# Kernel tuning notes

Hardware: AMD Instinct MI355X
Metric: run time of the kernel (lower is better)

Reference implementation:

```python
import jax, jax.numpy as jnp
import numpy as np

NEG = -1e20  # finite stand-in for -inf (exp underflows to 0; avoids nan grads)
S_RANGE = 19   # prune_range hard-coded in the module
TERM = 0       # termination/blank symbol
LM_ONLY = 0.25 # lm_only_scale; am_only_scale = 0 so that branch vanishes


def _mi(px, py):
    """RNN-T mutual-information forward DP (fast_rnnt mutual_information_recursion).
    px: (B,S,T+1) logprob of emitting symbol s+1 at (s,t); py: (B,S+1,T) blank logprobs.
    p[b,s,t] = logaddexp(p[b,s-1,t]+px[b,s-1,t], p[b,s,t-1]+py[b,s,t-1]); returns p[:,S,T]."""
    B, S, T1 = px.shape
    p0 = jnp.concatenate([jnp.zeros((B, 1), px.dtype),
                          jnp.cumsum(py[:, 0, :], axis=1)], axis=1)  # row s=0: (B,T+1)
    def outer(p_prev, inp):
        px_s, py_s = inp                 # (B,T+1), (B,T)
        b = p_prev + px_s                # vertical (emit) path into next row
        def inner(c, xs):
            b_t, py_t = xs
            c = jnp.logaddexp(b_t, c + py_t)
            return c, c
        _, rest = jax.lax.scan(inner, b[:, 0], (b[:, 1:].T, py_s.T))  # rest: (T,B)
        p_row = jnp.concatenate([b[:, :1], rest.T], axis=1)
        return p_row, None
    p_last, _ = jax.lax.scan(outer, p0,
                             (jnp.moveaxis(px, 1, 0), jnp.moveaxis(py[:, 1:, :], 1, 0)))
    return p_last[:, -1]  # (B,) total log-prob at (S,T)


def _smoothed_logprobs(am, lm, symbols):
    """fast_rnnt.get_rnnt_logprobs_smoothed with lm_only_scale=0.25, am_only_scale=0."""
    B, T, C = am.shape
    S = symbols.shape[1]
    lm_max = jnp.max(lm, axis=2, keepdims=True)   # (B,S+1,1)
    am_max = jnp.max(am, axis=2, keepdims=True)   # (B,T,1)
    lm_p = jnp.exp(lm - lm_max)
    am_p = jnp.exp(am - am_max)
    # normalizers[b,s,t] = log sum_k exp(lm[b,s,k] + am[b,t,k]) via matmul trick
    normalizers = jnp.log(jnp.einsum('bsc,btc->bst', lm_p, am_p)) \
        + lm_max + jnp.swapaxes(am_max, 1, 2)     # (B,S+1,T)
    sym_b = jnp.broadcast_to(symbols[:, None, :], (B, T, S))
    px_am = jnp.swapaxes(jnp.take_along_axis(am, sym_b, axis=2), 1, 2)  # (B,S,T)
    px_lm = jnp.take_along_axis(lm[:, :S], symbols[:, :, None], axis=2)  # (B,S,1)
    px = px_am + px_lm - normalizers[:, :S, :]
    lm_lsm = jax.nn.log_softmax(lm, axis=2)
    px_lmonly = jnp.take_along_axis(lm_lsm[:, :S], symbols[:, :, None], axis=2)
    comb = 1.0 - LM_ONLY
    px_i = comb * px + LM_ONLY * px_lmonly
    px_i = jnp.concatenate([px_i, jnp.full((B, S, 1), NEG, px_i.dtype)], axis=2)  # (B,S,T+1)
    py = am[:, :, TERM][:, None, :] + lm[:, :, TERM][:, :, None] - normalizers
    py_i = comb * py + LM_ONLY * lm_lsm[:, :, TERM][:, :, None]  # (B,S+1,T)
    return px_i, py_i


def _suffix_min(x):  # fast_rnnt _monotonic_lower_bound: x[t] = min(x[t:])
    return jax.lax.associative_scan(jnp.minimum, x, axis=1, reverse=True)


def _adjust_lower_bound(s_begin, r):  # fast_rnnt _adjust_pruning_lower_bound
    Tn = s_begin.shape[1]
    s_begin = _suffix_min(s_begin)
    off = (r - 1) * jnp.arange(Tn, dtype=s_begin.dtype)
    y = -(s_begin - off)
    y = jnp.maximum(_suffix_min(y), 0)
    return -(y - off)


def _prune_ranges(px_grad, py_grad, r):
    """fast_rnnt.get_rnnt_prune_ranges (all sequences full length)."""
    B, S, T1 = px_grad.shape
    T = T1 - 1
    py_pad = jnp.concatenate([py_grad, jnp.zeros((B, S + 1, 1), py_grad.dtype)], axis=2)
    tot = jnp.concatenate([px_grad, jnp.zeros((B, 1, T1), px_grad.dtype)], axis=1) + py_pad
    tot = jnp.concatenate([jnp.zeros((B, 1, T1), tot.dtype), tot], axis=1)  # (B,S+2,T1)
    cs = jnp.cumsum(tot, axis=1)
    diff = cs[:, r:, :] - cs[:, :-r, :]  # windowed occupancy sums
    s_begin = jnp.argmax(diff, axis=1)[:, :T].astype(jnp.int32)
    s_begin = _adjust_lower_bound(s_begin, r)
    return s_begin[:, :, None] + jnp.arange(r, dtype=jnp.int32)[None, None, :]  # (B,T,r)


def _pruned_logprobs(logits, symbols, ranges):
    """fast_rnnt.get_rnnt_logprobs_pruned."""
    B, T, r, C = logits.shape
    S = symbols.shape[1]
    norm = jax.nn.logsumexp(logits, axis=3)  # (B,T,r)
    sym_t = jnp.concatenate([symbols, jnp.full((B, 1), TERM, symbols.dtype)], axis=1)
    sym_b = jnp.broadcast_to(sym_t[:, None, :], (B, T, S + 1))
    pruned_sym = jnp.take_along_axis(sym_b, ranges, axis=2)  # (B,T,r)
    px = jnp.take_along_axis(logits, pruned_sym[..., None], axis=3)[..., 0] - norm
    py = logits[..., TERM] - norm
    def to_full(x):  # scatter (B,T,r) band into absolute symbol positions (B,T,S+1)
        pad = jnp.full((B, T, S + 1 - r), NEG, x.dtype)
        xf = jnp.concatenate([x, pad], axis=2)
        idx = (jnp.arange(S + 1)[None, None, :] - ranges[:, :, 0:1]) % (S + 1)
        return jnp.take_along_axis(xf, idx, axis=2)
    px_f = jnp.swapaxes(to_full(px), 1, 2)  # (B,S+1,T)
    py_f = jnp.swapaxes(to_full(py), 1, 2)  # (B,S+1,T)
    px_f = jnp.concatenate([px_f, jnp.full((B, S + 1, 1), NEG, px_f.dtype)], axis=2)[:, :S, :]
    return px_f, py_f  # (B,S,T+1), (B,S+1,T)


def _forward(am, lm, targets, joiner_w, joiner_b):
    px, py = _smoothed_logprobs(am, lm, targets)
    simple_loss = -jnp.mean(_mi(px, py))  # reduction='mean'
    # occupation-probability grads (values only, used for pruning)
    gpx, gpy = jax.grad(lambda a: jnp.sum(_mi(a[0], a[1])))(
        (jax.lax.stop_gradient(px), jax.lax.stop_gradient(py)))
    ranges = _prune_ranges(gpx, gpy, S_RANGE)  # (B,T,19) int32, constant wrt grads
    lm_pruned = jax.vmap(lambda l, rg: l[rg])(lm, ranges)  # (B,T,r,C) gather
    # joiner: logits = Linear(tanh(am_pruned + lm_pruned)); am broadcast over r
    logits = jnp.einsum('btrc,cd->btrd',
                        jnp.tanh(am[:, :, None, :] + lm_pruned), joiner_w) + joiner_b
    px2, py2 = _pruned_logprobs(logits.astype(jnp.float32), targets, ranges)
    pruned_loss = -jnp.mean(_mi(px2, py2))
    return 0.1 * simple_loss + pruned_loss


def setup_inputs() -> dict:
    key = jax.random.key(0)
    k = jax.random.split(key, 5)
    B, T, S, C = 8, 512, 128, 512
    return {
        "am": jax.random.normal(k[0], (B, T, C), jnp.float32),
        "lm": jax.random.normal(k[1], (B, S + 1, C), jnp.float32),
        "targets": jax.random.randint(k[2], (B, S), 1, C),  # blank=0 excluded
        "y_lens": jnp.full((B,), S, jnp.int32),             # full-length boundaries
        "joiner_w": 0.05 * jax.random.normal(k[3], (C, C), jnp.float32),
        "joiner_b": jnp.zeros((C,), jnp.float32),
    }


def reference(am, lm, targets, y_lens, joiner_w, joiner_b):
    # boundary = [0, 0, y_lens(=S), T] for every sequence
    return _forward(am, lm, targets, joiner_w, joiner_b)
```

## Files before the change

### kernel.cpp

```cpp
#include <hip/hip_runtime.h>
#include <math.h>

#define NEGV -1e20f
#define DPAD 132
#define RBOFF 16
#define ROWSA 676
#define RB(p,b) ((p) + ((size_t)(b) * ROWSA + RBOFF) * DPAD)
#define NROWS 77824

typedef __attribute__((ext_vector_type(4))) float floatx4;
typedef __attribute__((ext_vector_type(8))) short short8;


__device__ __forceinline__ float lae(float a, float b){
  float mx = fmaxf(a, b);
  float mn = fminf(a, b);
  return mx + __logf(1.f + __expf(mn - mx));
}

__device__ __forceinline__ short f2bf(float x){
  union { float f; unsigned u; } v; v.f = x;
  unsigned r = v.u + 0x7fffu + ((v.u >> 16) & 1u);
  return (short)(r >> 16);
}

__device__ __forceinline__ float tanh5(float x){
  float e = __expf(2.f * x);
  return 1.f - 2.f * __builtin_amdgcn_rcpf(e + 1.f);
}

__global__ __launch_bounds__(256) void k_row_stats(
    const float* __restrict__ in, float* __restrict__ outMax, float* __restrict__ outLse)
{
  int row = blockIdx.x;
  const float* r = in + (size_t)row * 512;
  int tid = threadIdx.x;
  float v0 = r[tid], v1 = r[tid + 256];
  float m = fmaxf(v0, v1);
  #pragma unroll
  for (int off = 32; off; off >>= 1) m = fmaxf(m, __shfl_xor(m, off, 64));
  __shared__ float sm[4];
  __shared__ float sbm;
  int wv = tid >> 6;
  if ((tid & 63) == 0) sm[wv] = m;
  __syncthreads();
  if (tid == 0) sbm = fmaxf(fmaxf(sm[0], sm[1]), fmaxf(sm[2], sm[3]));
  __syncthreads();
  float mx = sbm;
  if (tid == 0) outMax[row] = mx;
  if (outLse){
    float s = __expf(v0 - mx) + __expf(v1 - mx);
    #pragma unroll
    for (int off = 32; off; off >>= 1) s += __shfl_xor(s, off, 64);
    __shared__ float sp[4];
    if ((tid & 63) == 0) sp[wv] = s;
    __syncthreads();
    if (tid == 0) outLse[row] = mx + __logf(sp[0] + sp[1] + sp[2] + sp[3]);
  }
}

__global__ __launch_bounds__(256) void k_wb(const float* __restrict__ W, short* __restrict__ Wb){
  int idx = blockIdx.x * 256 + threadIdx.x;
  int d = idx >> 9, c = idx & 511;
  Wb[idx] = f2bf(W[c * 512 + d]);
}

__global__ __launch_bounds__(256) void k_norm(
    const float* __restrict__ am, const float* __restrict__ lm,
    const float* __restrict__ lmMax, const float* __restrict__ amMax,
    float* __restrict__ normv)
{
  int b = blockIdx.z;
  int s0 = blockIdx.y * 16;
  int t0 = blockIdx.x * 128;
  __shared__ float lmS[16][68];
  __shared__ float amS[128][68];
  int tid = threadIdx.x;
  int ts = tid >> 4, tt = tid & 15;
  float acc[8];
  #pragma unroll
  for (int j = 0; j < 8; ++j) acc[j] = 0.f;

  for (int k0 = 0; k0 < 512; k0 += 64){
    {
      int e = tid * 4;
      int rr = e >> 6, cc = e & 63;
      int s = s0 + rr;
      floatx4 o = {0.f, 0.f, 0.f, 0.f};
      if (s < 129){
        float mx = lmMax[b * 129 + s];
        floatx4 v = *(const floatx4*)(lm + ((size_t)(b * 129 + s)) * 512 + k0 + cc);
        o[0] = __expf(v[0] - mx); o[1] = __expf(v[1] - mx);
        o[2] = __expf(v[2] - mx); o[3] = __expf(v[3] - mx);
      }
      *(floatx4*)&lmS[rr][cc] = o;
    }
    #pragma unroll
    for (int i = 0; i < 8; ++i){
      int e = (tid + i * 256) * 4;
      int rr = e >> 6, cc = e & 63;
      float mx = amMax[b * 512 + t0 + rr];
      floatx4 v = *(const floatx4*)(am + ((size_t)(b * 512 + t0 + rr)) * 512 + k0 + cc);
      floatx4 o;
      o[0] = __expf(v[0] - mx); o[1] = __expf(v[1] - mx);
      o[2] = __expf(v[2] - mx); o[3] = __expf(v[3] - mx);
      *(floatx4*)&amS[rr][cc] = o;
    }
    __syncthreads();
    #pragma unroll 4
    for (int k = 0; k < 64; ++k){
      float a = lmS[ts][k];
      #pragma unroll
      for (int j = 0; j < 8; ++j) acc[j] += a * amS[tt + 16 * j][k];
    }
    __syncthreads();
  }
  int s = s0 + ts;
  if (s < 129){
    float lmx = lmMax[b * 129 + s];
    #pragma unroll
    for (int j = 0; j < 8; ++j){
      int t = t0 + tt + 16 * j;
      normv[((size_t)(b * 129 + s)) * 512 + t] = __logf(acc[j]) + lmx + amMax[b * 512 + t];
    }
  }
}

__global__ __launch_bounds__(256) void k_pxpy(
    const float* __restrict__ am, const float* __restrict__ lm,
    const int* __restrict__ targets, const float* __restrict__ normv,
    const float* __restrict__ lmLse, float* __restrict__ pxd, float* __restrict__ pyd)
{
  int bs = blockIdx.x;
  int b = bs / 129, s = bs % 129;
  float lm0 = lm[(size_t)bs * 512];
  float lse = lmLse[bs];
  int sym = 0; float lms = 0.f;
  if (s < 128){ sym = targets[b * 128 + s]; lms = lm[(size_t)bs * 512 + sym]; }
  const float* nrm = normv + (size_t)bs * 512;
  float* pydb = RB(pyd, b);
  float* pxdb = RB(pxd, b);
  for (int t = threadIdx.x; t < 513; t += 256){
    if (t < 512){
      float n = nrm[t];
      float a0 = am[((size_t)(b * 512 + t)) * 512];
      pydb[(size_t)(s + t) * DPAD + s] = 0.75f * (a0 + lm0 - n) + 0.25f * (lm0 - lse);
      if (s < 128){
        float as = am[((size_t)(b * 512 + t)) * 512 + sym];
        pxdb[(size_t)(s + t) * DPAD + s] = 0.75f * (as + lms - n) + 0.25f * (lms - lse);
      }
    } else if (s < 128){
      pxdb[(size_t)(s + 512) * DPAD + s] = NEGV;
    }
  }
}


__device__ __forceinline__ void dp_fwd_run(
    const float* __restrict__ pxb, const float* __restrict__ pyb,
    float* __restrict__ pab, float* __restrict__ tot, int b)
{
  int l = threadIdx.x;
  const int a = 2 * l;
  float curA = NEGV, curB = NEGV, curC = NEGV, send = NEGV;
  int paddr = (l - 1) << 2;

  float2 cpx = *(const float2*)(pxb - DPAD + a);
  float2 cpy = *(const float2*)(pyb - DPAD + a);
  float  cpz = pyb[-DPAD + 128];

  float2 b0px[8], b0py[8], b1px[8], b1py[8];
  float  b0pz[8], b1pz[8];
  float  outx[8], outy[8], outc[8];

  #pragma unroll
  for (int j = 0; j < 8; ++j){
    b0px[j] = *(const float2*)(pxb + (size_t)j * DPAD + a);
    b0py[j] = *(const float2*)(pyb + (size_t)j * DPAD + a);
    b0pz[j] = pyb[(size_t)j * DPAD + 128];
  }

  for (int i = 0; i < 40; ++i){
    int d0 = i * 16;
    #pragma unroll
    for (int j = 0; j < 8; ++j){
      b1px[j] = *(const float2*)(pxb + (size_t)(d0 + 8 + j) * DPAD + a);
      b1py[j] = *(const float2*)(pyb + (size_t)(d0 + 8 + j) * DPAD + a);
      b1pz[j] = pyb[(size_t)(d0 + 8 + j) * DPAD + 128];
    }
    #pragma unroll
    for (int j = 0; j < 8; ++j){
      int d = d0 + j;
      float2 pxm = j ? b0px[j - 1] : cpx;
      float2 pym = j ? b0py[j - 1] : cpy;
      float  pzm = j ? b0pz[j - 1] : cpz;
      float recv = __int_as_float(
          __builtin_amdgcn_ds_bpermute(paddr, __float_as_int(send)));
      int tA = d - a, tC = d - 128;
      float aaA = (l > 0) ? recv : NEGV;
      float bbA = (tA >= 1) ? curA + pym.x : NEGV;
      float nvA = lae(aaA, bbA);
      if (l == 0 && d == 0) nvA = 0.f;
      float aaB = curA + pxm.x;
      float bbB = (tA >= 2) ? curB + pym.y : NEGV;
      float nvB = lae(aaB, bbB);
      float aaC = curB + pxm.y;
      float bbC = (tC >= 1) ? curC + pzm : NEGV;
      float nvC = lae(aaC, bbC);
      if (tA >= 0 && tA <= 512) curA = nvA;
      if (tA >= 1 && tA <= 513) curB = nvB;
      if (tC >= 0 && tC <= 512) curC = nvC;
      send = curB + b0px[j].y;
      outx[j] = curA; outy[j] = curB; outc[j] = curC;
    }
    cpx = b0px[7]; cpy = b0py[7]; cpz = b0pz[7];
    if (pab){
      #pragma unroll
      for (int j = 0; j < 8; ++j)
        *(float2*)(pab + (size_t)(d0 + j) * DPAD + a) = make_float2(outx[j], outy[j]);
      if (l == 63){
        #pragma unroll
        for (int j = 0; j < 8; ++j)
          pab[(size_t)(d0 + j) * DPAD + 128] = outc[j];
      }
    }
    #pragma unroll
    for (int j = 0; j < 8; ++j){
      b0px[j] = *(const float2*)(pxb + (size_t)(d0 + 16 + j) * DPAD + a);
      b0py[j] = *(const float2*)(pyb + (size_t)(d0 + 16 + j) * DPAD + a);
      b0pz[j] = pyb[(size_t)(d0 + 16 + j) * DPAD + 128];
    }
    #pragma unroll
    for (int j = 0; j < 8; ++j){
      int d = d0 + 8 + j;
      float2 pxm = j ? b1px[j - 1] : cpx;
      float2 pym = j ? b1py[j - 1] : cpy;
      float  pzm = j ? b1pz[j - 1] : cpz;
      float recv = __int_as_float(
          __builtin_amdgcn_ds_bpermute(paddr, __float_as_int(send)));
      int tA = d - a, tC = d - 128;
      float aaA = (l > 0) ? recv : NEGV;
      float bbA = (tA >= 1) ? curA + pym.x : NEGV;
      float nvA = lae(aaA, bbA);
      float aaB = curA + pxm.x;
      float bbB = (tA >= 2) ? curB + pym.y : NEGV;
      float nvB = lae(aaB, bbB);
      float aaC = curB + pxm.y;
      float bbC = (tC >= 1) ? curC + pzm : NEGV;
      float nvC = lae(aaC, bbC);
      if (tA >= 0 && tA <= 512) curA = nvA;
      if (tA >= 1 && tA <= 513) curB = nvB;
      if (tC >= 0 && tC <= 512) curC = nvC;
      send = curB + b1px[j].y;
      outx[j] = curA; outy[j] = curB; outc[j] = curC;
    }
    cpx = b1px[7]; cpy = b1py[7]; cpz = b1pz[7];
    if (pab){
      #pragma unroll
      for (int j = 0; j < 8; ++j)
        *(float2*)(pab + (size_t)(d0 + 8 + j) * DPAD + a) = make_float2(outx[j], outy[j]);
      if (l == 63){
        #pragma unroll
        for (int j = 0; j < 8; ++j)
          pab[(size_t)(d0 + 8 + j) * DPAD + 128] = outc[j];
      }
    }
  }
  {
    float aaC = curB + cpx.y;
    float bbC = curC + cpz;
    curC = lae(aaC, bbC);
    if (l == 63){
      if (pab) pab[(size_t)640 * DPAD + 128] = curC;
      tot[b] = curC;
    }
  }
}

__device__ __forceinline__ void dp_bwd_run(
    const float* __restrict__ pxb, const float* __restrict__ pyb,
    float* __restrict__ beb)
{
  int l = threadIdx.x;
  const int a = 2 * l;
  float curA = NEGV, curB = NEGV, curC = NEGV, send = NEGV;
  int paddr = (l + 1) << 2;

  float2 b0px[8], b0py[8], b1px[8], b1py[8];
  float  b0pz[8], b1pz[8];
  float  outx[8], outy[8], outc[8];

  #pragma unroll
  for (int j = 0; j < 8; ++j){
    b0px[j] = *(const float2*)(pxb + (size_t)(640 - j) * DPAD + a);
    b0py[j] = *(const float2*)(pyb + (size_t)(640 - j) * DPAD + a);
    b0pz[j] = pyb[(size_t)(640 - j) * DPAD + 128];
  }

  for (int i = 0; i < 40; ++i){
    int d0 = 640 - 16 * i;
    #pragma unroll
    for (int j = 0; j < 8; ++j){
      b1px[j] = *(const float2*)(pxb + (size_t)(d0 - 8 - j) * DPAD + a);
      b1py[j] = *(const float2*)(pyb + (size_t)(d0 - 8 - j) * DPAD + a);
      b1pz[j] = pyb[(size_t)(d0 - 8 - j) * DPAD + 128];
    }
    #pragma unroll
    for (int j = 0; j < 8; ++j){
      int d = d0 - j;
      float2 pxA = b0px[j]; float2 pyA = b0py[j]; float pzA = b0pz[j];
      float recv = __int_as_float(
          __builtin_amdgcn_ds_bpermute(paddr, __float_as_int(send)));
      int tA = d - a, tB = tA - 1, tC = d - 128;
      float aaA = pxA.x + curB;
      float bbA = (tA <= 511) ? pyA.x + curA : NEGV;
      float nvA = lae(aaA, bbA);
      float up = (l < 63) ? recv : curC;
      float aaB = pxA.y + up;
      float bbB = (tB <= 511) ? pyA.y + curB : NEGV;
      float nvB = lae(aaB, bbB);
      float nvC = (tC <= 511) ? pzA + curC : NEGV;
      if (tC == 512) nvC = 0.f;
      if (tA >= 0 && tA <= 512) curA = nvA;
      if (tB >= 0 && tB <= 512) curB = nvB;
      if (tC >= 0 && tC <= 512) curC = nvC;
      send = curA;
      outx[j] = curA; outy[j] = curB; outc[j] = curC;
    }
    #pragma unroll
    for (int j = 0; j < 8; ++j)
      *(float2*)(beb + (size_t)(d0 - j) * DPAD + a) = make_float2(outx[j], outy[j]);
    if (l == 63){
      #pragma unroll
      for (int j = 0; j < 8; ++j)
        beb[(size_t)(d0 - j) * DPAD + 128] = outc[j];
    }
    #pragma unroll
    for (int j = 0; j < 8; ++j){
      b0px[j] = *(const float2*)(pxb + (size_t)(d0 - 16 - j) * DPAD + a);
      b0py[j] = *(const float2*)(pyb + (size_t)(d0 - 16 - j) * DPAD + a);
      b0pz[j] = pyb[(size_t)(d0 - 16 - j) * DPAD + 128];
    }
    #pragma unroll
    for (int j = 0; j < 8; ++j){
      int d = d0 - 8 - j;
      float2 pxA = b1px[j]; float2 pyA = b1py[j]; float pzA = b1pz[j];
      float recv = __int_as_float(
          __builtin_amdgcn_ds_bpermute(paddr, __float_as_int(send)));
      int tA = d - a, tB = tA - 1, tC = d - 128;
      float aaA = pxA.x + curB;
      float bbA = (tA <= 511) ? pyA.x + curA : NEGV;
      float nvA = lae(aaA, bbA);
      float up = (l < 63) ? recv : curC;
      float aaB = pxA.y + up;
      float bbB = (tB <= 511) ? pyA.y + curB : NEGV;
      float nvB = lae(aaB, bbB);
      float nvC = (tC <= 511) ? pzA + curC : NEGV;
      if (tC == 512) nvC = 0.f;
      if (tA >= 0 && tA <= 512) curA = nvA;
      if (tB >= 0 && tB <= 512) curB = nvB;
      if (tC >= 0 && tC <= 512) curC = nvC;
      send = curA;
      outx[j] = curA; outy[j] = curB; outc[j] = curC;
    }
    #pragma unroll
    for (int j = 0; j < 8; ++j)
      *(float2*)(beb + (size_t)(d0 - 8 - j) * DPAD + a) = make_float2(outx[j], outy[j]);
    if (l == 63){
      #pragma unroll
      for (int j = 0; j < 8; ++j)
        beb[(size_t)(d0 - 8 - j) * DPAD + 128] = outc[j];
    }
  }
  {
    float2 pxA = b0px[0]; float2 pyA = b0py[0];
    float recv = __int_as_float(
        __builtin_amdgcn_ds_bpermute(paddr, __float_as_int(send)));
    int tA = -a, tB = tA - 1;
    float aaA = pxA.x + curB;
    float bbA = (tA <= 511) ? pyA.x + curA : NEGV;
    float nvA = lae(aaA, bbA);
    float up = (l < 63) ? recv : curC;
    float aaB = pxA.y + up;
    float bbB = (tB <= 511) ? pyA.y + curB : NEGV;
    float nvB = lae(aaB, bbB);
    if (tA >= 0 && tA <= 512) curA = nvA;
    if (tB >= 0 && tB <= 512) curB = nvB;
    *(float2*)(beb + a) = make_float2(curA, curB);
    if (l == 63) beb[128] = curC;
  }
}

__global__ __launch_bounds__(64) void k_dp_fb(
    const float* __restrict__ pxd, const float* __restrict__ pyd,
    float* __restrict__ pad, float* __restrict__ betad, float* __restrict__ tots)
{
  int blk = blockIdx.x;
  if (blk < 8){
    int b = blk;
    dp_fwd_run(RB(pxd, b), RB(pyd, b), RB(pad, b), tots, b);
  } else {
    int b = blk - 8;
    dp_bwd_run(RB(pxd, b), RB(pyd, b), RB(betad, b));
  }
}

__global__ __launch_bounds__(64) void k_dp_f2(
    const float* __restrict__ pxd, const float* __restrict__ pyd,
    float* __restrict__ totp)
{
  int b = blockIdx.x;
  dp_fwd_run(RB(pxd, b), RB(pyd, b), (float*)nullptr, totp, b);
}

__global__ __launch_bounds__(256) void k_window(
    const float* __restrict__ pxd, const float* __restrict__ pyd,
    const float* __restrict__ pad, const float* __restrict__ betad,
    const float* __restrict__ tots, int* __restrict__ sbr)
{
  __shared__ float tote[129][66];
  int b = blockIdx.x >> 3;
  int t0 = (blockIdx.x & 7) << 6;
  const float* px = RB(pxd, b);
  const float* py = RB(pyd, b);
  const float* pa = RB(pad, b);
  const float* be = RB(betad, b);
  float tv = tots[b];
  int tid = threadIdx.x;
  int wv = tid >> 6, ln = tid & 63;
  for (int dd = wv; dd < 192; dd += 4){
    int d = t0 + dd;
    int slo = dd - 63 > 0 ? dd - 63 : 0;
    int shi = dd < 128 ? dd : 128;
    int s = slo + ln;
    if (s <= shi){
      size_t r0 = (size_t)d * DPAD + s, r1 = (size_t)(d + 1) * DPAD + s;
      float pav = pa[r0];
      float v = __expf(pav + py[r0] + be[r1] - tv);
      if (s < 128) v += __expf(pav + px[r0] + be[r1 + 1] - tv);
      tote[s][dd - s] = v;
    }
  }
  __syncthreads();
  if (tid < 64){
    int c = tid;
    float win = 0.f;
    for (int s = 0; s < 19; ++s) win += tote[s][c];
    float best = win; int arg = 0;
    for (int w2 = 1; w2 <= 110; ++w2){
      win += tote[w2 + 18][c] - tote[w2 - 1][c];
      if (win > best){ best = win; arg = w2; }
    }
    sbr[b * 512 + t0 + c] = arg;
  }
}

__global__ void k_adjust(const int* __restrict__ sbr, int* __restrict__ sbeg){
  if (threadIdx.x != 0) return;
  int b = blockIdx.x;
  const int* in = sbr + b * 512;
  int* out = sbeg + b * 512;
  int sbm = 1 << 30, ym = 1 << 30;
  for (int t = 511; t >= 0; --t){
    sbm = min(sbm, in[t]);
    int y = 18 * t - sbm;
    ym = min(ym, y);
    int yc = ym > 0 ? ym : 0;
    out[t] = 18 * t - yc;
  }
}

__global__ __launch_bounds__(256) void k_stageH(
    const float* __restrict__ am, const float* __restrict__ lm,
    const int* __restrict__ sbeg, short* __restrict__ Hb)
{
  __shared__ int rowAm[64], rowLm[64];
  int tid = threadIdx.x;
  int r0 = blockIdx.x * 64;
  if (tid < 64){
    int row = r0 + tid;
    int g = row / 19;
    int j = row - g * 19;
    int b = g >> 9, t = g & 511;
    int sidx = sbeg[b * 512 + t] + j;
    rowAm[tid] = (b * 512 + t) * 512;
    rowLm[tid] = (b * 129 + sidx) * 512;
  }
  __syncthreads();
  int row = tid >> 2;
  int kb = (tid & 3) * 8;
  const float* ap = am + (size_t)rowAm[row];
  const float* lp = lm + (size_t)rowLm[row];
  short* hp = Hb + (size_t)(r0 + row) * 512;
  #pragma unroll 4
  for (int i = 0; i < 16; ++i){
    int k = kb + i * 32;
    floatx4 a0 = *(const floatx4*)(ap + k);
    floatx4 a1 = *(const floatx4*)(ap + k + 4);
    floatx4 l0 = *(const floatx4*)(lp + k);
    floatx4 l1 = *(const floatx4*)(lp + k + 4);
    short8 h;
    h[0] = f2bf(tanh5(a0[0] + l0[0]));
    h[1] = f2bf(tanh5(a0[1] + l0[1]));
    h[2] = f2bf(tanh5(a0[2] + l0[2]));
    h[3] = f2bf(tanh5(a0[3] + l0[3]));
    h[4] = f2bf(tanh5(a1[0] + l1[0]));
    h[5] = f2bf(tanh5(a1[1] + l1[1]));
    h[6] = f2bf(tanh5(a1[2] + l1[2]));
    h[7] = f2bf(tanh5(a1[3] + l1[3]));
    *(short8*)(hp + k) = h;
  }
}

__global__ __launch_bounds__(256) void k_jgemm(
    const short* __restrict__ Hb, const short* __restrict__ Wb,
    const float* __restrict__ bias, const int* __restrict__ targets,
    const int* __restrict__ sbeg,
    float2* __restrict__ pms, float* __restrict__ pxraw, float* __restrict__ pyraw)
{
  __shared__ int rowSym[128];
  __shared__ float redM[128][2];
  __shared__ float redS[128][2];
  __shared__ float rowM[128];

  int tid = threadIdx.x;
  int rt = blockIdx.x;
  int nb = blockIdx.y;
  int r0 = rt * 128, c0 = nb * 128;
  if (tid < 128){
    int row = r0 + tid;
    int g = row / 19;
    int j = row - g * 19;
    int b = g >> 9, t = g & 511;
    int sidx = sbeg[b * 512 + t] + j;
    rowSym[tid] = (sidx < 128) ? targets[b * 128 + sidx] : 0;
  }
  __syncthreads();

  int w = tid >> 6, lane = tid & 63, q = lane >> 4, ln = lane & 15;
  int mBase = (w & 1) * 64;
  int nBase = (w >> 1) * 64;
  const short* Ab = Hb + (size_t)(r0 + mBase + ln) * 512 + q * 8;
  const short* Bb = Wb + (size_t)(c0 + nBase + ln) * 512 + q * 8;

  floatx4 acc[4][4];
  #pragma unroll
  for (int mt = 0; mt < 4; ++mt)
    #pragma unroll
    for (int nt = 0; nt < 4; ++nt) acc[mt][nt] = (floatx4){0.f, 0.f, 0.f, 0.f};

  #pragma unroll 2
  for (int k0 = 0; k0 < 512; k0 += 32){
    short8 af[4], bf[4];
    #pragma unroll
    for (int mt = 0; mt < 4; ++mt)
      af[mt] = *(const short8*)(Ab + (size_t)mt * 16 * 512 + k0);
    #pragma unroll
    for (int nt = 0; nt < 4; ++nt)
      bf[nt] = *(const short8*)(Bb + (size_t)nt * 16 * 512 + k0);
    #pragma unroll
    for (int nt = 0; nt < 4; ++nt)
      #pragma unroll
      for (int mt = 0; mt < 4; ++mt)
        acc[mt][nt] = __builtin_amdgcn_mfma_f32_16x16x32_bf16(af[mt], bf[nt], acc[mt][nt], 0, 0, 0);
  }

  #pragma unroll
  for (int nt = 0; nt < 4; ++nt){
    int col = c0 + nBase + nt * 16 + ln;
    float bc = bias[col];
    #pragma unroll
    for (int mt = 0; mt < 4; ++mt)
      #pragma unroll
      for (int r = 0; r < 4; ++r){
        float v = acc[mt][nt][r] + bc;
        acc[mt][nt][r] = v;
        int rl = mBase + mt * 16 + q * 4 + r;
        if (col == 0) pyraw[r0 + rl] = v;
        if (col == rowSym[rl]) pxraw[r0 + rl] = v;
      }
  }
  #pragma unroll
  for (int mt = 0; mt < 4; ++mt)
    #pragma unroll
    for (int r = 0; r < 4; ++r){
      int rl = mBase + mt * 16 + q * 4 + r;
      float m = acc[mt][0][r];
      #pragma unroll
      for (int nt = 1; nt < 4; ++nt) m = fmaxf(m, acc[mt][nt][r]);
      m = fmaxf(m, __shfl_xor(m, 1, 16));
      m = fmaxf(m, __shfl_xor(m, 2, 16));
      m = fmaxf(m, __shfl_xor(m, 4, 16));
      m = fmaxf(m, __shfl_xor(m, 8, 16));
      if (ln == 0) redM[rl][w >> 1] = m;
    }
  __syncthreads();
  if (tid < 128) rowM[tid] = fmaxf(redM[tid][0], redM[tid][1]);
  __syncthreads();
  #pragma unroll
  for (int mt = 0; mt < 4; ++mt)
    #pragma unroll
    for (int r = 0; r < 4; ++r){
      int rl = mBase + mt * 16 + q * 4 + r;
      float rm = rowM[rl];
      float sa = 0.f;
      #pragma unroll
      for (int nt = 0; nt < 4; ++nt) sa += __expf(acc[mt][nt][r] - rm);
      sa += __shfl_xor(sa, 1, 16);
      sa += __shfl_xor(sa, 2, 16);
      sa += __shfl_xor(sa, 4, 16);
      sa += __shfl_xor(sa, 8, 16);
      if (ln == 0) redS[rl][w >> 1] = sa;
    }
  __syncthreads();
  if (tid < 128)
    pms[(size_t)nb * NROWS + r0 + tid] = make_float2(rowM[tid], redS[tid][0] + redS[tid][1]);
}

__global__ __launch_bounds__(256) void k_jfin(
    const float2* __restrict__ pms, const float* __restrict__ pxraw,
    const float* __restrict__ pyraw, float* __restrict__ pxv, float* __restrict__ pyv)
{
  int row = blockIdx.x * 256 + threadIdx.x;
  float2 p0 = pms[row];
  float2 p1 = pms[NROWS + row];
  float2 p2 = pms[2 * NROWS + row];
  float2 p3 = pms[3 * NROWS + row];
  float M = fmaxf(fmaxf(p0.x, p1.x), fmaxf(p2.x, p3.x));
  float S = p0.y * __expf(p0.x - M) + p1.y * __expf(p1.x - M)
          + p2.y * __expf(p2.x - M) + p3.y * __expf(p3.x - M);
  float norm = M + __logf(S);
  pxv[row] = pxraw[row] - norm;
  pyv[row] = pyraw[row] - norm;
}

__global__ __launch_bounds__(192) void k_band(
    const float* __restrict__ pxv, const float* __restrict__ pyv,
    const int* __restrict__ sbeg, float* __restrict__ px2d, float* __restrict__ py2d)
{
  int bd = blockIdx.x;
  int b = bd / 640, d = bd - b * 640;
  int s = threadIdx.x;
  int t = d - s;
  if (s > 128 || t < 0 || t > 512) return;
  size_t addr = ((size_t)b * ROWSA + RBOFF + d) * DPAD + s;
  if (s < 128){
    float v;
    if (t == 512) v = NEGV;
    else {
      int start = sbeg[b * 512 + t];
      int j = s - start;
      v = (j >= 0 && j < 19) ? pxv[((size_t)(b * 512 + t)) * 19 + j] : NEGV;
    }
    px2d[addr] = v;
  }
  if (t <= 511){
    int start = sbeg[b * 512 + t];
    int j = s - start;
    py2d[addr] = (j >= 0 && j < 19) ? pyv[((size_t)(b * 512 + t)) * 19 + j] : NEGV;
  }
}

__global__ void k_final(const float* __restrict__ tots, const float* __restrict__ totp,
                        float* __restrict__ out){
  if (blockIdx.x == 0 && threadIdx.x == 0){
    float a = 0.f, c = 0.f;
    for (int i = 0; i < 8; ++i){ a += tots[i]; c += totp[i]; }
    out[0] = -0.1f * (a * 0.125f) - (c * 0.125f);
  }
}

extern "C" void kernel_launch(void* const* d_in, const int* in_sizes, int n_in,
                              void* d_out, int out_size, void* d_ws, size_t ws_size,
                              hipStream_t stream){
  (void)in_sizes; (void)n_in; (void)out_size; (void)ws_size;
  const float* am      = (const float*)d_in[0];
  const float* lm      = (const float*)d_in[1];
  const int*   targets = (const int*)d_in[2];
  const float* W       = (const float*)d_in[4];
  const float* bias    = (const float*)d_in[5];
  float* out = (float*)d_out;

  char* base = (char*)d_ws;
  size_t off = 0;
  auto alloc = [&](size_t bytes) -> char* {
    char* r = base + off;
    off += (bytes + 255) & ~(size_t)255;
    return r;
  };
  const size_t DARR = 8ull * ROWSA * DPAD * 4;
  float* amMax = (float*)alloc(8ull * 512 * 4);
  float* lmMax = (float*)alloc(8ull * 129 * 4);
  float* lmLse = (float*)alloc(8ull * 129 * 4);
  float* normv = (float*)alloc(8ull * 129 * 512 * 4);
  float* pxd   = (float*)alloc(DARR);
  float* pyd   = (float*)alloc(DARR);
  float* pad   = (float*)alloc(DARR);
  float* betad = (float*)alloc(DARR);
  float* tots  = (float*)alloc(8 * 4);
  float* totp  = (float*)alloc(8 * 4);
  int*   sbr   = (int*)alloc(8ull * 512 * 4);
  int*   sbeg  = (int*)alloc(8ull * 512 * 4);
  float* pxv   = (float*)alloc((size_t)NROWS * 4);
  float* pyv   = (float*)alloc((size_t)NROWS * 4);
  short* Wb    = (short*)alloc(512ull * 512 * 2);
  short* Hb    = (short*)alloc((size_t)NROWS * 512 * 2);
  float2* pms  = (float2*)alloc(4ull * NROWS * 8);
  float* pxraw = (float*)alloc((size_t)NROWS * 4);
  float* pyraw = (float*)alloc((size_t)NROWS * 4);
  float* px2d  = pxd;
  float* py2d  = pyd;

  k_row_stats<<<dim3(4096), dim3(256), 0, stream>>>(am, amMax, (float*)nullptr);
  k_row_stats<<<dim3(1032), dim3(256), 0, stream>>>(lm, lmMax, lmLse);
  k_wb<<<dim3(1024), dim3(256), 0, stream>>>(W, Wb);
  k_norm<<<dim3(4, 9, 8), dim3(256), 0, stream>>>(am, lm, lmMax, amMax, normv);
  k_pxpy<<<dim3(1032), dim3(256), 0, stream>>>(am, lm, targets, normv, lmLse, pxd, pyd);
  k_dp_fb<<<dim3(16), dim3(64), 0, stream>>>(pxd, pyd, pad, betad, tots);
  k_window<<<dim3(64), dim3(256), 0, stream>>>(pxd, pyd, pad, betad, tots, sbr);
  k_adjust<<<dim3(8), dim3(64), 0, stream>>>(sbr, sbeg);
  k_stageH<<<dim3(1216), dim3(256), 0, stream>>>(am, lm, sbeg, Hb);
  k_jgemm<<<dim3(608, 4), dim3(256), 0, stream>>>(Hb, Wb, bias, targets, sbeg, pms, pxraw, pyraw);
  k_jfin<<<dim3(304), dim3(256), 0, stream>>>(pms, pxraw, pyraw, pxv, pyv);
  k_band<<<dim3(5120), dim3(192), 0, stream>>>(pxv, pyv, sbeg, px2d, py2d);
  k_dp_f2<<<dim3(8), dim3(64), 0, stream>>>(px2d, py2d, totp);
  k_final<<<dim3(1), dim3(64), 0, stream>>>(tots, totp, out);
}
```

Measured before the change: 646.8 us.

## Stage joiner GEMM tiles through LDS via direct global-to-LDS loads, remap blocks per XCD

The joiner GEMM now copies each 128x32 A and B tile into shared memory with global_load_lds, then reads MFMA fragments from LDS instead of issuing strided global loads per wave. The 2D grid becomes a 1D grid whose block index is remapped so that consecutive row tiles and all four column blocks land on the same XCD, which should improve L2 reuse. The K loop is not double-buffered, so every step has two barriers and a load stall. Because the LDS tiles use a 32-short row stride with no padding, the fragment reads may hit bank conflicts.

```diff
diff --git a/kernel.cpp b/kernel.cpp
--- a/kernel.cpp
+++ b/kernel.cpp
@@ -27,6 +27,13 @@
 __device__ __forceinline__ float tanh5(float x){
   float e = __expf(2.f * x);
   return 1.f - 2.f * __builtin_amdgcn_rcpf(e + 1.f);
+}
+
+__device__ __forceinline__ void gl_lds16(const short* __restrict__ g, short* l){
+  __builtin_amdgcn_global_load_lds(
+      (const __attribute__((address_space(1))) unsigned int*)g,
+      (__attribute__((address_space(3))) unsigned int*)(unsigned long long)l,
+      16, 0, 0);
 }
 
 __global__ __launch_bounds__(256) void k_row_stats(
@@ -518,15 +525,20 @@
     const int* __restrict__ sbeg,
     float2* __restrict__ pms, float* __restrict__ pxraw, float* __restrict__ pyraw)
 {
+  __shared__ short As[128 * 32];
+  __shared__ short Bs[128 * 32];
   __shared__ int rowSym[128];
   __shared__ float redM[128][2];
   __shared__ float redS[128][2];
   __shared__ float rowM[128];
 
   int tid = threadIdx.x;
-  int rt = blockIdx.x;
-  int nb = blockIdx.y;
+  int bid = blockIdx.x;
+  int xcd = bid & 7, idx = bid >> 3;
+  int nb = idx & 3;
+  int rt = xcd * 76 + (idx >> 2);
   int r0 = rt * 128, c0 = nb * 128;
+
   if (tid < 128){
     int row = r0 + tid;
     int g = row / 19;
@@ -535,13 +547,21 @@
     int sidx = sbeg[b * 512 + t] + j;
     rowSym[tid] = (sidx < 128) ? targets[b * 128 + sidx] : 0;
   }
-  __syncthreads();
 
   int w = tid >> 6, lane = tid & 63, q = lane >> 4, ln = lane & 15;
   int mBase = (w & 1) * 64;
   int nBase = (w >> 1) * 64;
-  const short* Ab = Hb + (size_t)(r0 + mBase + ln) * 512 + q * 8;
-  const short* Bb = Wb + (size_t)(c0 + nBase + ln) * 512 + q * 8;
+
+  int sg0 = (w * 2) * 64 + lane;
+  int sRow0 = sg0 >> 2, sKp0 = (sg0 & 3) << 3;
+  int sg1 = sg0 + 64;
+  int sRow1 = sg1 >> 2, sKp1 = (sg1 & 3) << 3;
+  const short* Ag = Hb + (size_t)r0 * 512;
+  const short* Bg = Wb + (size_t)c0 * 512;
+  short* AsB0 = As + (w * 2) * 512;
+  short* AsB1 = As + (w * 2 + 1) * 512;
+  short* BsB0 = Bs + (w * 2) * 512;
+  short* BsB1 = Bs + (w * 2 + 1) * 512;
 
   floatx4 acc[4][4];
   #pragma unroll
@@ -549,15 +569,20 @@
     #pragma unroll
     for (int nt = 0; nt < 4; ++nt) acc[mt][nt] = (floatx4){0.f, 0.f, 0.f, 0.f};
 
-  #pragma unroll 2
   for (int k0 = 0; k0 < 512; k0 += 32){
+    gl_lds16(Ag + (size_t)sRow0 * 512 + k0 + sKp0, AsB0);
+    gl_lds16(Ag + (size_t)sRow1 * 512 + k0 + sKp1, AsB1);
+    gl_lds16(Bg + (size_t)sRow0 * 512 + k0 + sKp0, BsB0);
+    gl_lds16(Bg + (size_t)sRow1 * 512 + k0 + sKp1, BsB1);
+    __syncthreads();
     short8 af[4], bf[4];
     #pragma unroll
     for (int mt = 0; mt < 4; ++mt)
-      af[mt] = *(const short8*)(Ab + (size_t)mt * 16 * 512 + k0);
+      af[mt] = *(const short8*)&As[(mBase + mt * 16 + ln) * 32 + q * 8];
     #pragma unroll
     for (int nt = 0; nt < 4; ++nt)
-      bf[nt] = *(const short8*)(Bb + (size_t)nt * 16 * 512 + k0);
+      bf[nt] = *(const short8*)&Bs[(nBase + nt * 16 + ln) * 32 + q * 8];
+    __syncthreads();
     #pragma unroll
     for (int nt = 0; nt < 4; ++nt)
       #pragma unroll
@@ -703,8 +728,8 @@
   int*   sbeg  = (int*)alloc(8ull * 512 * 4);
   float* pxv   = (float*)alloc((size_t)NROWS * 4);
   float* pyv   = (float*)alloc((size_t)NROWS * 4);
-  short* Wb    = (short*)alloc(512ull * 512 * 2);
-  short* Hb    = (short*)alloc((size_t)NROWS * 512 * 2);
+  short* Wb    = (short*)alloc((512ull * 512 + 512) * 2);
+  short* Hb    = (short*)alloc(((size_t)NROWS * 512 + 512) * 2);
   float2* pms  = (float2*)alloc(4ull * NROWS * 8);
   float* pxraw = (float*)alloc((size_t)NROWS * 4);
   float* pyraw = (float*)alloc((size_t)NROWS * 4);
@@ -720,7 +745,7 @@
   k_window<<<dim3(64), dim3(256), 0, stream>>>(pxd, pyd, pad, betad, tots, sbr);
   k_adjust<<<dim3(8), dim3(64), 0, stream>>>(sbr, sbeg);
   k_stageH<<<dim3(1216), dim3(256), 0, stream>>>(am, lm, sbeg, Hb);
-  k_jgemm<<<dim3(608, 4), dim3(256), 0, stream>>>(Hb, Wb, bias, targets, sbeg, pms, pxraw, pyraw);
+  k_jgemm<<<dim3(2432), dim3(256), 0, stream>>>(Hb, Wb, bias, targets, sbeg, pms, pxraw, pyraw);
   k_jfin<<<dim3(304), dim3(256), 0, stream>>>(pms, pxraw, pyraw, pxv, pyv);
   k_band<<<dim3(5120), dim3(192), 0, stream>>>(pxv, pyv, sbeg, px2d, py2d);
   k_dp_f2<<<dim3(8), dim3(64), 0, stream>>>(px2d, py2d, totp);
```

After: 554.7 us. 1.17x faster.
